# Kernel tuning notes

Hardware: AMD Instinct MI355X
Metric: run time of the kernel (lower is better)

Reference implementation:

```python
import jax, jax.numpy as jnp
import numpy as np

HIDDEN = 1024
N_ROUTED = 16
N_SHARED = 2
TOP_K = 2
MID_R = HIDDEN // 4   # routed_ratio=4 -> 256
MID_S = HIDDEN // 2   # shared_ratio=2 -> 512


def setup_inputs() -> dict:
    key = jax.random.key(0)
    ks = jax.random.split(key, 8)
    s = 0.02
    return {
        "x": jax.random.normal(ks[0], (2, 1024, HIDDEN), dtype=jnp.float32),
        "router_w": jax.random.normal(ks[1], (HIDDEN, N_ROUTED), dtype=jnp.float32) * s,
        "wg_r": jax.random.normal(ks[2], (N_ROUTED, HIDDEN, MID_R), dtype=jnp.float32) * s,
        "wu_r": jax.random.normal(ks[3], (N_ROUTED, HIDDEN, MID_R), dtype=jnp.float32) * s,
        "wd_r": jax.random.normal(ks[4], (N_ROUTED, MID_R, HIDDEN), dtype=jnp.float32) * s,
        "wg_s": jax.random.normal(ks[5], (N_SHARED, HIDDEN, MID_S), dtype=jnp.float32) * s,
        "wu_s": jax.random.normal(ks[6], (N_SHARED, HIDDEN, MID_S), dtype=jnp.float32) * s,
        "wd_s": jax.random.normal(ks[7], (N_SHARED, MID_S, HIDDEN), dtype=jnp.float32) * s,
    }


def reference(x, router_w, wg_r, wu_r, wd_r, wg_s, wu_s, wd_s):
    orig_shape = x.shape
    flat = x.reshape(-1, orig_shape[-1])  # [T, D]

    # ---- shared experts: sum of always-active SwiGLU FFNs ----
    gs = jnp.einsum("td,ndm->tnm", flat, wg_s)            # [T, Ns, Ms]
    us = jnp.einsum("td,ndm->tnm", flat, wu_s)
    out = jnp.einsum("tnm,nmd->td", jax.nn.silu(gs) * us, wd_s)  # summed over n

    # ---- router: softmax -> top-k -> renormalize ----
    logits = (flat @ router_w).astype(jnp.float32)        # [T, E]
    probs = jax.nn.softmax(logits, axis=-1)
    weights, indices = jax.lax.top_k(probs, TOP_K)        # [T, K]
    weights = weights / (weights.sum(axis=-1, keepdims=True) + 1e-9)
    weights = weights.astype(x.dtype)

    # combine weights as dense [T, E] (top-k indices are distinct)
    comb = jnp.sum(jax.nn.one_hot(indices, N_ROUTED, dtype=x.dtype)
                   * weights[..., None], axis=1)          # [T, E]

    # ---- routed experts (dense dispatch; combine folded into hidden) ----
    g = jnp.einsum("td,edm->tem", flat, wg_r)             # [T, E, Mr]
    u = jnp.einsum("td,edm->tem", flat, wu_r)
    h = jax.nn.silu(g) * u                                 # [T, E, Mr]
    h = h * comb[:, :, None]                               # weight before down-proj (linear)
    out = out + jnp.einsum("tem,emd->td", h, wd_r)

    return out.reshape(orig_shape)
```

## Files before the change

### kernel.cpp

```cpp
#include <hip/hip_runtime.h>
#include <hip/hip_bf16.h>
#include <stdint.h>

#define T_TOK 2048
#define DHID  1024
#define NEXP  16
#define MR    256
#define MS    512
#define CAP   512

typedef float  f32x4  __attribute__((ext_vector_type(4)));
typedef __bf16 bf16x8 __attribute__((ext_vector_type(8)));

typedef __attribute__((address_space(3))) void       lds_void;
typedef const __attribute__((address_space(1))) void gbl_void;

#define GLOAD16(g, l) __builtin_amdgcn_global_load_lds((gbl_void*)(g), (lds_void*)(l), 16, 0, 0)

__device__ __forceinline__ ushort f2bf(float f) {
  uint32_t u = __float_as_uint(f);
  u = (u + 0x7fffu + ((u >> 16) & 1u)) >> 16;
  return (ushort)u;
}
__device__ __forceinline__ float bf2f(ushort v) { return __uint_as_float(((uint32_t)v) << 16); }

__device__ __forceinline__ void stage128(const ushort* __restrict__ g0, int strideE,
                                         ushort* lds, int tid) {
  const int wave = tid >> 6;
  const int r = tid >> 3, colE = (tid & 7) * 8;
#pragma unroll
  for (int s = 0; s < 4; ++s) {
    const int row = s * 32 + r;
    GLOAD16(g0 + (size_t)row * strideE + (colE ^ ((row & 7) << 3)), lds + s * 2048 + wave * 512);
  }
}

__device__ __forceinline__ void stage_gather128(const ushort* __restrict__ xb,
                                                const int tok[4], int k0,
                                                ushort* lds, int tid) {
  const int wave = tid >> 6;
  const int r = tid >> 3, colE = (tid & 7) * 8;
#pragma unroll
  for (int s = 0; s < 4; ++s) {
    const int row = s * 32 + r;
    GLOAD16(xb + (size_t)tok[s] * DHID + k0 + (colE ^ ((row & 7) << 3)), lds + s * 2048 + wave * 512);
  }
}

__device__ __forceinline__ void mfma_tile(const ushort* a_sh, const ushort* b_sh,
                                          int wr, int wc, int lane, f32x4 (&acc)[4][4]) {
  const int rb = lane & 15;
  const int sw = (rb & 7) << 3;
#pragma unroll
  for (int kk = 0; kk < 64; kk += 32) {
    const int k8 = (kk + ((lane >> 4) << 3)) ^ sw;
    bf16x8 af[4];
#pragma unroll
    for (int m = 0; m < 4; m++)
      af[m] = *(const bf16x8*)&a_sh[(wr * 64 + m * 16 + rb) * 64 + k8];
#pragma unroll
    for (int n = 0; n < 4; n++) {
      bf16x8 bf = *(const bf16x8*)&b_sh[(wc * 64 + n * 16 + rb) * 64 + k8];
#pragma unroll
      for (int m = 0; m < 4; m++)
        acc[m][n] = __builtin_amdgcn_mfma_f32_16x16x32_bf16(af[m], bf, acc[m][n], 0, 0, 0);
    }
  }
}

__device__ __forceinline__ bool queue_lookup(const int* __restrict__ cnt, int mti,
                                             int& e_out, int& s0_out, int& c_out) {
  int acc = 0;
#pragma unroll
  for (int ee = 0; ee < NEXP; ++ee) {
    const int c = cnt[ee];
    const int ntl = (c + 127) >> 7;
    if (mti < acc + ntl) { e_out = ee; s0_out = (mti - acc) << 7; c_out = c; return true; }
    acc += ntl;
  }
  return false;
}

struct TP {
  const float* in; ushort* out;
  int R, C, out_ld, ilv;
  long long out_batch;
};

__device__ __forceinline__ void tpose_tile(const TP p, int local, void* smem, int tid) {
  float (*t_sh)[65] = (float(*)[65])smem;
  const int tr = p.R >> 6, tc = p.C >> 6, per = tr * tc;
  const int b = local / per, rem = local - b * per;
  const int rt = rem / tc, ct = rem - rt * tc;
  const int r0 = rt * 64, c0 = ct * 64;
  const float* ip = p.in + (size_t)b * p.R * p.C;
  ushort* op = p.out + (size_t)b * p.out_batch;
  const int trd = tid >> 4, tcd = (tid & 15) * 4;
#pragma unroll
  for (int q = 0; q < 4; q++) {
    float4 v = *(const float4*)&ip[(size_t)(r0 + trd + q * 16) * p.C + c0 + tcd];
    t_sh[trd + q * 16][tcd + 0] = v.x; t_sh[trd + q * 16][tcd + 1] = v.y;
    t_sh[trd + q * 16][tcd + 2] = v.z; t_sh[trd + q * 16][tcd + 3] = v.w;
  }
  __syncthreads();
#pragma unroll
  for (int q = 0; q < 4; q++) {
    const int cc = trd + q * 16;
    int rr = c0 + cc;
    if (p.ilv) rr = ((rr >> 4) << 5) + (rr & 15);
    ushort4 o;
    o.x = f2bf(t_sh[tcd + 0][cc]); o.y = f2bf(t_sh[tcd + 1][cc]);
    o.z = f2bf(t_sh[tcd + 2][cc]); o.w = f2bf(t_sh[tcd + 3][cc]);
    *(ushort4*)&op[(size_t)rr * p.out_ld + r0 + tcd] = o;
  }
}

__global__ __launch_bounds__(256) void k_prep(
    const float* __restrict__ x, const float* __restrict__ rw,
    ushort* __restrict__ xb, int* __restrict__ topi, float2* __restrict__ topw)
{
  __shared__ float rw_sh[NEXP][DHID];
  const int tid = threadIdx.x;
#pragma unroll
  for (int it = 0; it < 16; ++it) {
    const int flat = it * 1024 + tid * 4;
    float4 v = *(const float4*)&rw[flat];
    const int d = flat >> 4, e = flat & 15;
    rw_sh[e + 0][d] = v.x; rw_sh[e + 1][d] = v.y;
    rw_sh[e + 2][d] = v.z; rw_sh[e + 3][d] = v.w;
  }
  __syncthreads();

  const int wave = tid >> 6, lane = tid & 63;
  for (int tk = 0; tk < 2; ++tk) {
    const int t = blockIdx.x * 8 + wave * 2 + tk;
    const float* xp = x + (size_t)t * DHID;
    float acc[NEXP];
#pragma unroll
    for (int e = 0; e < NEXP; e++) acc[e] = 0.f;
#pragma unroll
    for (int i = 0; i < 4; ++i) {
      const int d4 = i * 64 + lane;
      float4 xv = *(const float4*)&xp[d4 * 4];
      ushort4 o; o.x = f2bf(xv.x); o.y = f2bf(xv.y); o.z = f2bf(xv.z); o.w = f2bf(xv.w);
      *(ushort4*)&xb[(size_t)t * DHID + d4 * 4] = o;
#pragma unroll
      for (int e = 0; e < NEXP; e++) {
        float4 wv = *(const float4*)&rw_sh[e][d4 * 4];
        acc[e] = fmaf(xv.x, wv.x, acc[e]);
        acc[e] = fmaf(xv.y, wv.y, acc[e]);
        acc[e] = fmaf(xv.z, wv.z, acc[e]);
        acc[e] = fmaf(xv.w, wv.w, acc[e]);
      }
    }
#pragma unroll
    for (int off = 32; off >= 1; off >>= 1) {
#pragma unroll
      for (int e = 0; e < NEXP; e++) acc[e] += __shfl_xor(acc[e], off, 64);
    }
    if (lane == 0) {
      float m = acc[0];
#pragma unroll
      for (int e = 1; e < NEXP; e++) m = fmaxf(m, acc[e]);
      float p[NEXP], Z = 0.f;
#pragma unroll
      for (int e = 0; e < NEXP; e++) { p[e] = __expf(acc[e] - m); Z += p[e]; }
      const float inv = 1.f / Z;
      int i1 = 0; float p1 = p[0] * inv;
      for (int e = 1; e < NEXP; e++) { float pe = p[e] * inv; if (pe > p1) { p1 = pe; i1 = e; } }
      int i2 = -1; float p2 = -1.f;
      for (int e = 0; e < NEXP; e++) { if (e == i1) continue; float pe = p[e] * inv; if (pe > p2) { p2 = pe; i2 = e; } }
      const float denom = p1 + p2 + 1e-9f;
      topi[t] = i1 | (i2 << 8);
      topw[t] = make_float2(p1 / denom, p2 / denom);
    }
  }
}

__global__ __launch_bounds__(256) void k_build_tp(
    const int* __restrict__ topi, const float2* __restrict__ topw,
    int* __restrict__ cnt, int* __restrict__ ltok, float* __restrict__ lw,
    int* __restrict__ tslot, TP t0, TP t1, TP t2, TP t3)
{
  __shared__ float t_smem[64][65];
  const int tid = threadIdx.x;
  const int bid = blockIdx.x;
  if (bid >= NEXP) {
    const int local = bid - NEXP;
    if      (local < 1024) tpose_tile(t0, local,        t_smem, tid);
    else if (local < 2048) tpose_tile(t1, local - 1024, t_smem, tid);
    else if (local < 2304) tpose_tile(t2, local - 2048, t_smem, tid);
    else                   tpose_tile(t3, local - 2304, t_smem, tid);
    return;
  }
  int* wsum = (int*)t_smem;
  const int e = bid;
  const int wave = tid >> 6, lane = tid & 63;
  const int t0i = tid * 8;

  int4 a = *(const int4*)&topi[t0i];
  int4 b = *(const int4*)&topi[t0i + 4];
  int ti[8] = {a.x, a.y, a.z, a.w, b.x, b.y, b.z, b.w};
  int match[8]; int c = 0;
#pragma unroll
  for (int k = 0; k < 8; ++k) {
    const int i1 = ti[k] & 0xff, i2 = (ti[k] >> 8) & 0xff;
    match[k] = (i1 == e) ? 1 : ((i2 == e) ? 2 : 0);
    c += (match[k] != 0);
  }
  int incl = c;
#pragma unroll
  for (int off = 1; off < 64; off <<= 1) {
    int n = __shfl_up(incl, off, 64);
    if (lane >= off) incl += n;
  }
  if (lane == 63) wsum[wave] = incl;
  __syncthreads();
  int base = incl - c;
  for (int w = 0; w < wave; ++w) base += wsum[w];
  if (tid == 0) {
    int tot = wsum[0] + wsum[1] + wsum[2] + wsum[3];
    cnt[e] = tot > CAP ? CAP : tot;
  }
#pragma unroll
  for (int k = 0; k < 8; ++k) {
    if (match[k]) {
      const int t = t0i + k;
      if (base < CAP) {
        float2 w2 = topw[t];
        ltok[e * CAP + base] = t;
        lw[e * CAP + base] = (match[k] == 1) ? w2.x : w2.y;
        tslot[t * 2 + (match[k] - 1)] = e * CAP + base;
      } else {
        tslot[t * 2 + (match[k] - 1)] = -1;
      }
      base++;
    }
  }
}

__global__ __launch_bounds__(256) void k_up(
    const ushort* __restrict__ xb, const ushort* __restrict__ wguTs,
    const ushort* __restrict__ wguTr, const int* __restrict__ cnt,
    const int* __restrict__ ltok, const float* __restrict__ lw,
    ushort* __restrict__ h_s, ushort* __restrict__ h_r, TP t4, TP t5)
{
  __shared__ ushort smem[2 * 128 * 64];
  ushort* a_sh = smem;
  ushort* b_sh = smem + 128 * 64;
  ushort (*r_sh)[64] = (ushort(*)[64])smem;
  const int tid = threadIdx.x, lane = tid & 63, wave = tid >> 6;
  const int wr = wave >> 1, wc = wave & 1;
  const int rb = lane & 15, rowoff = (lane >> 4) << 2;
  const int bid0 = blockIdx.x;
  if (bid0 >= 512) {
    const int local = bid0 - 512;
    if (local < 1024) tpose_tile(t4, local, smem, tid);
    else              tpose_tile(t5, local - 1024, smem, tid);
    return;
  }
  f32x4 acc[4][4] = {};

  if (bid0 < 256) {
    const int bid = (bid0 & 7) * 32 + (bid0 >> 3);
    const int mt = bid & 15, nt = bid >> 4;
    const ushort* Ab = xb + (size_t)mt * 128 * DHID;
    const ushort* Bb = wguTs + (size_t)nt * 128 * DHID;
    for (int k0 = 0; k0 < DHID; k0 += 64) {
      __syncthreads();
      stage128(Ab + k0, DHID, a_sh, tid);
      stage128(Bb + k0, DHID, b_sh, tid);
      __syncthreads();
      mfma_tile(a_sh, b_sh, wr, wc, lane, acc);
    }
    __syncthreads();
#pragma unroll
    for (int m = 0; m < 4; m++)
#pragma unroll
      for (int p = 0; p < 2; p++) {
        f32x4 g = acc[m][2 * p], u = acc[m][2 * p + 1];
#pragma unroll
        for (int jj = 0; jj < 4; jj++) {
          float gv = g[jj];
          float hv = (gv / (1.f + __expf(-gv))) * u[jj];
          r_sh[wr * 64 + m * 16 + rowoff + jj][wc * 32 + p * 16 + rb] = f2bf(hv);
        }
      }
    __syncthreads();
#pragma unroll
    for (int sp = 0; sp < 4; sp++) {
      const int row = sp * 32 + (tid >> 3), col = (tid & 7) * 8;
      *(uint4*)&h_s[(size_t)(mt * 128 + row) * DHID + nt * 64 + col] = *(const uint4*)&r_sh[row][col];
    }
  } else {
    const int id = bid0 - 256;
    const int mti = id >> 2, ntile = id & 3;
    int e, s0, c;
    if (!queue_lookup(cnt, mti, e, s0, c)) return;
    int tok[4];
#pragma unroll
    for (int s = 0; s < 4; ++s) {
      int slot = s0 + s * 32 + (tid >> 3);
      if (slot >= c) slot = c - 1;
      tok[s] = ltok[e * CAP + slot];
    }
    const ushort* Bb = wguTr + ((size_t)e * 512 + ntile * 128) * DHID;
    for (int k0 = 0; k0 < DHID; k0 += 64) {
      __syncthreads();
      stage_gather128(xb, tok, k0, a_sh, tid);
      stage128(Bb + k0, DHID, b_sh, tid);
      __syncthreads();
      mfma_tile(a_sh, b_sh, wr, wc, lane, acc);
    }
    __syncthreads();
#pragma unroll
    for (int m = 0; m < 4; m++)
#pragma unroll
      for (int jj = 0; jj < 4; jj++) {
        const int slot = s0 + wr * 64 + m * 16 + rowoff + jj;
        const float w = (slot < c) ? lw[e * CAP + slot] : 0.f;
#pragma unroll
        for (int p = 0; p < 2; p++) {
          float gv = acc[m][2 * p][jj];
          float hv = (gv / (1.f + __expf(-gv))) * acc[m][2 * p + 1][jj] * w;
          r_sh[wr * 64 + m * 16 + rowoff + jj][wc * 32 + p * 16 + rb] = f2bf(hv);
        }
      }
    __syncthreads();
#pragma unroll
    for (int sp = 0; sp < 4; sp++) {
      const int row = sp * 32 + (tid >> 3), col = (tid & 7) * 8;
      *(uint4*)&h_r[((size_t)e * CAP + s0 + row) * MR + ntile * 64 + col] = *(const uint4*)&r_sh[row][col];
    }
  }
}

__global__ __launch_bounds__(256) void k_down(
    const ushort* __restrict__ h_s, const ushort* __restrict__ wdTs,
    const ushort* __restrict__ h_r, const ushort* __restrict__ wdTr,
    const int* __restrict__ cnt, ushort* __restrict__ ds, ushort* __restrict__ dr)
{
  __shared__ ushort smem[2 * 128 * 64];
  ushort* a_sh = smem;
  ushort* b_sh = smem + 128 * 64;
  ushort (*r2)[128] = (ushort(*)[128])smem;
  const int tid = threadIdx.x, lane = tid & 63, wave = tid >> 6;
  const int wr = wave >> 1, wc = wave & 1;
  const int rb = lane & 15, rowoff = (lane >> 4) << 2;
  f32x4 acc[4][4] = {};
  const int bid0 = blockIdx.x;

  const ushort* Ab; const ushort* Bb;
  int K, rowbase, colbase; ushort* outp;
  if (bid0 < 128) {
    const int bid = (bid0 & 7) * 16 + (bid0 >> 3);
    const int mt = bid >> 3, nt = bid & 7;
    Ab = h_s + (size_t)mt * 128 * DHID;
    Bb = wdTs + (size_t)nt * 128 * DHID;
    K = DHID; rowbase = mt * 128; colbase = nt * 128;
    outp = ds;
  } else {
    const int id = bid0 - 128;
    const int mti = id >> 3, nt = id & 7;
    int e, s0, c;
    if (!queue_lookup(cnt, mti, e, s0, c)) return;
    Ab = h_r + ((size_t)e * CAP + s0) * MR;
    Bb = wdTr + ((size_t)e * DHID + nt * 128) * MR;
    K = MR; rowbase = e * CAP + s0; colbase = nt * 128;
    outp = dr;
  }
  for (int k0 = 0; k0 < K; k0 += 64) {
    __syncthreads();
    stage128(Ab + k0, K, a_sh, tid);
    stage128(Bb + k0, K, b_sh, tid);
    __syncthreads();
    mfma_tile(a_sh, b_sh, wr, wc, lane, acc);
  }
  __syncthreads();
#pragma unroll
  for (int m = 0; m < 4; m++)
#pragma unroll
    for (int n = 0; n < 4; n++) {
      f32x4 v = acc[m][n];
#pragma unroll
      for (int jj = 0; jj < 4; jj++)
        r2[wr * 64 + m * 16 + rowoff + jj][wc * 64 + n * 16 + rb] = f2bf(v[jj]);
    }
  __syncthreads();
  {
    const int row = tid >> 1, colE = (tid & 1) * 64;
    ushort* op = &outp[(size_t)(rowbase + row) * DHID + colbase + colE];
#pragma unroll
    for (int q = 0; q < 8; q++)
      *(uint4*)(op + q * 8) = *(const uint4*)&r2[row][colE + q * 8];
  }
}

__global__ __launch_bounds__(256) void k_comb(
    const ushort* __restrict__ ds, const ushort* __restrict__ dr,
    const int* __restrict__ tslot, float* __restrict__ out)
{
  const int tid = threadIdx.x;
  const int t = blockIdx.x * 2 + (tid >> 7);
  const int d = (tid & 127) * 8;
  const int es1 = tslot[t * 2], es2 = tslot[t * 2 + 1];
  uint4 a = *(const uint4*)&ds[(size_t)t * DHID + d];
  float r[8];
  const ushort* ap = (const ushort*)&a;
#pragma unroll
  for (int k = 0; k < 8; ++k) r[k] = bf2f(ap[k]);
  if (es1 >= 0) {
    uint4 b = *(const uint4*)&dr[(size_t)es1 * DHID + d];
    const ushort* bp = (const ushort*)&b;
#pragma unroll
    for (int k = 0; k < 8; ++k) r[k] += bf2f(bp[k]);
  }
  if (es2 >= 0) {
    uint4 b = *(const uint4*)&dr[(size_t)es2 * DHID + d];
    const ushort* bp = (const ushort*)&b;
#pragma unroll
    for (int k = 0; k < 8; ++k) r[k] += bf2f(bp[k]);
  }
  float4* op = (float4*)&out[(size_t)t * DHID + d];
  op[0] = make_float4(r[0], r[1], r[2], r[3]);
  op[1] = make_float4(r[4], r[5], r[6], r[7]);
}

extern "C" void kernel_launch(void* const* d_in, const int* in_sizes, int n_in,
                              void* d_out, int out_size, void* d_ws, size_t ws_size,
                              hipStream_t stream) {
  const float* x    = (const float*)d_in[0];
  const float* rw   = (const float*)d_in[1];
  const float* wg_r = (const float*)d_in[2];
  const float* wu_r = (const float*)d_in[3];
  const float* wd_r = (const float*)d_in[4];
  const float* wg_s = (const float*)d_in[5];
  const float* wu_s = (const float*)d_in[6];
  const float* wd_s = (const float*)d_in[7];
  float* out = (float*)d_out;

  char* ws = (char*)d_ws;
  size_t off = 0;
  ushort* xb    = (ushort*)(ws + off); off += (size_t)T_TOK * DHID * 2;
  ushort* wguTs = (ushort*)(ws + off); off += (size_t)2048 * DHID * 2;
  ushort* wdTs  = (ushort*)(ws + off); off += (size_t)DHID * DHID * 2;
  ushort* wguTr = (ushort*)(ws + off); off += (size_t)NEXP * 512 * DHID * 2;
  ushort* wdTr  = (ushort*)(ws + off); off += (size_t)NEXP * DHID * MR * 2;
  ushort* h_s   = (ushort*)(ws + off); off += (size_t)T_TOK * DHID * 2;
  ushort* h_r   = (ushort*)(ws + off); off += (size_t)NEXP * CAP * MR * 2;
  ushort* ds    = (ushort*)(ws + off); off += (size_t)T_TOK * DHID * 2;
  ushort* dr    = (ushort*)(ws + off); off += (size_t)NEXP * CAP * DHID * 2;
  int*    cnt   = (int*)(ws + off);    off += 256;
  int*    ltok  = (int*)(ws + off);    off += (size_t)NEXP * CAP * 4;
  float*  lw    = (float*)(ws + off);  off += (size_t)NEXP * CAP * 4;
  int*    topi  = (int*)(ws + off);    off += (size_t)T_TOK * 4;
  float2* topw  = (float2*)(ws + off); off += (size_t)T_TOK * 8;
  int*    tslot = (int*)(ws + off);    off += (size_t)T_TOK * 2 * 4;
  if (off > ws_size) return;

  TP t0 = {wg_r, wguTr,             DHID, MR,   DHID, 1, (long long)512 * DHID};
  TP t1 = {wu_r, wguTr + 16 * DHID, DHID, MR,   DHID, 1, (long long)512 * DHID};
  TP t2 = {wg_s, wguTs,             DHID, MS,   DHID, 1, (long long)1024 * DHID};
  TP t3 = {wu_s, wguTs + 16 * DHID, DHID, MS,   DHID, 1, (long long)1024 * DHID};
  TP t4 = {wd_r, wdTr,              MR,   DHID, MR,   0, (long long)DHID * MR};
  TP t5 = {wd_s, wdTs,              MS,   DHID, DHID, 0, (long long)MS};

  k_prep<<<T_TOK / 8, 256, 0, stream>>>(x, rw, xb, topi, topw);
  k_build_tp<<<NEXP + 2560, 256, 0, stream>>>(topi, topw, cnt, ltok, lw, tslot, t0, t1, t2, t3);
  k_up<<<512 + 1280, 256, 0, stream>>>(xb, wguTs, wguTr, cnt, ltok, lw, h_s, h_r, t4, t5);
  k_down<<<640, 256, 0, stream>>>(h_s, wdTs, h_r, wdTr, cnt, ds, dr);
  k_comb<<<T_TOK / 2, 256, 0, stream>>>(ds, dr, tslot, out);
}
```

Before: 85.19 us.

## Double-buffer LDS staging with async prefetch in up and down GEMM kernels

After: 75.99 us. 10.8% less time.

```diff
diff --git a/kernel.cpp b/kernel.cpp
--- a/kernel.cpp
+++ b/kernel.cpp
@@ -16,6 +16,15 @@
 typedef const __attribute__((address_space(1))) void gbl_void;
 
 #define GLOAD16(g, l) __builtin_amdgcn_global_load_lds((gbl_void*)(g), (lds_void*)(l), 16, 0, 0)
+#define VMCNT8() asm volatile("s_waitcnt vmcnt(8)" ::: "memory")
+#define VMCNT0() asm volatile("s_waitcnt vmcnt(0)" ::: "memory")
+#define SCHED_FENCE() __builtin_amdgcn_sched_barrier(0)
+
+__device__ __forceinline__ void barrier_raw() {
+  asm volatile("" ::: "memory");
+  __builtin_amdgcn_s_barrier();
+  asm volatile("" ::: "memory");
+}
 
 __device__ __forceinline__ ushort f2bf(float f) {
   uint32_t u = __float_as_uint(f);
@@ -245,9 +254,7 @@
     const int* __restrict__ ltok, const float* __restrict__ lw,
     ushort* __restrict__ h_s, ushort* __restrict__ h_r, TP t4, TP t5)
 {
-  __shared__ ushort smem[2 * 128 * 64];
-  ushort* a_sh = smem;
-  ushort* b_sh = smem + 128 * 64;
+  __shared__ ushort smem[4 * 128 * 64];
   ushort (*r_sh)[64] = (ushort(*)[64])smem;
   const int tid = threadIdx.x, lane = tid & 63, wave = tid >> 6;
   const int wr = wave >> 1, wc = wave & 1;
@@ -266,14 +273,27 @@
     const int mt = bid & 15, nt = bid >> 4;
     const ushort* Ab = xb + (size_t)mt * 128 * DHID;
     const ushort* Bb = wguTs + (size_t)nt * 128 * DHID;
-    for (int k0 = 0; k0 < DHID; k0 += 64) {
-      __syncthreads();
-      stage128(Ab + k0, DHID, a_sh, tid);
-      stage128(Bb + k0, DHID, b_sh, tid);
-      __syncthreads();
-      mfma_tile(a_sh, b_sh, wr, wc, lane, acc);
-    }
-    __syncthreads();
+    stage128(Ab, DHID, smem, tid);
+    stage128(Bb, DHID, smem + 16384, tid);
+    for (int t = 0; t < 16; ++t) {
+      const int co = (t & 1) * 8192;
+      const int no = ((t + 1) & 1) * 8192;
+      if (t < 15) {
+        stage128(Ab + (t + 1) * 64, DHID, smem + no, tid);
+        stage128(Bb + (t + 1) * 64, DHID, smem + 16384 + no, tid);
+        SCHED_FENCE();
+        VMCNT8();
+      } else {
+        SCHED_FENCE();
+        VMCNT0();
+      }
+      SCHED_FENCE();
+      barrier_raw();
+      SCHED_FENCE();
+      mfma_tile(smem + co, smem + 16384 + co, wr, wc, lane, acc);
+      SCHED_FENCE();
+      barrier_raw();
+    }
 #pragma unroll
     for (int m = 0; m < 4; m++)
 #pragma unroll
@@ -305,14 +325,27 @@
       tok[s] = ltok[e * CAP + slot];
     }
     const ushort* Bb = wguTr + ((size_t)e * 512 + ntile * 128) * DHID;
-    for (int k0 = 0; k0 < DHID; k0 += 64) {
-      __syncthreads();
-      stage_gather128(xb, tok, k0, a_sh, tid);
-      stage128(Bb + k0, DHID, b_sh, tid);
-      __syncthreads();
-      mfma_tile(a_sh, b_sh, wr, wc, lane, acc);
-    }
-    __syncthreads();
+    stage_gather128(xb, tok, 0, smem, tid);
+    stage128(Bb, DHID, smem + 16384, tid);
+    for (int t = 0; t < 16; ++t) {
+      const int co = (t & 1) * 8192;
+      const int no = ((t + 1) & 1) * 8192;
+      if (t < 15) {
+        stage_gather128(xb, tok, (t + 1) * 64, smem + no, tid);
+        stage128(Bb + (t + 1) * 64, DHID, smem + 16384 + no, tid);
+        SCHED_FENCE();
+        VMCNT8();
+      } else {
+        SCHED_FENCE();
+        VMCNT0();
+      }
+      SCHED_FENCE();
+      barrier_raw();
+      SCHED_FENCE();
+      mfma_tile(smem + co, smem + 16384 + co, wr, wc, lane, acc);
+      SCHED_FENCE();
+      barrier_raw();
+    }
 #pragma unroll
     for (int m = 0; m < 4; m++)
 #pragma unroll
@@ -340,9 +373,7 @@
     const ushort* __restrict__ h_r, const ushort* __restrict__ wdTr,
     const int* __restrict__ cnt, ushort* __restrict__ ds, ushort* __restrict__ dr)
 {
-  __shared__ ushort smem[2 * 128 * 64];
-  ushort* a_sh = smem;
-  ushort* b_sh = smem + 128 * 64;
+  __shared__ ushort smem[4 * 128 * 64];
   ushort (*r2)[128] = (ushort(*)[128])smem;
   const int tid = threadIdx.x, lane = tid & 63, wave = tid >> 6;
   const int wr = wave >> 1, wc = wave & 1;
@@ -369,14 +400,28 @@
     K = MR; rowbase = e * CAP + s0; colbase = nt * 128;
     outp = dr;
   }
-  for (int k0 = 0; k0 < K; k0 += 64) {
-    __syncthreads();
-    stage128(Ab + k0, K, a_sh, tid);
-    stage128(Bb + k0, K, b_sh, tid);
-    __syncthreads();
-    mfma_tile(a_sh, b_sh, wr, wc, lane, acc);
-  }
-  __syncthreads();
+  const int nk = K >> 6;
+  stage128(Ab, K, smem, tid);
+  stage128(Bb, K, smem + 16384, tid);
+  for (int t = 0; t < nk; ++t) {
+    const int co = (t & 1) * 8192;
+    const int no = ((t + 1) & 1) * 8192;
+    if (t + 1 < nk) {
+      stage128(Ab + (t + 1) * 64, K, smem + no, tid);
+      stage128(Bb + (t + 1) * 64, K, smem + 16384 + no, tid);
+      SCHED_FENCE();
+      VMCNT8();
+    } else {
+      SCHED_FENCE();
+      VMCNT0();
+    }
+    SCHED_FENCE();
+    barrier_raw();
+    SCHED_FENCE();
+    mfma_tile(smem + co, smem + 16384 + co, wr, wc, lane, acc);
+    SCHED_FENCE();
+    barrier_raw();
+  }
 #pragma unroll
   for (int m = 0; m < 4; m++)
 #pragma unroll
```
